# Optimization experiments

Measured on AMD Instinct MI355X. Metric: run time of the kernel, lower is better.

The kernel has to match this reference:

```python
import jax, jax.numpy as jnp
import numpy as np
import math

MAX_P = 150
D_MODEL = 128
N_HEADS = 4
D_HEAD = D_MODEL // N_HEADS
D_MLP = 512
D_MEM = 64
VOCAB = MAX_P + 2  # 152
EQ_TOKEN = MAX_P + 1  # 151
B = 65536


def setup_inputs() -> dict:
    key = jax.random.key(0)
    ks = jax.random.split(key, 20)
    s = 1.0 / math.sqrt(D_MODEL)
    inp = {
        "p_val": jax.random.randint(ks[0], (B,), 0, MAX_P),
        "a": jax.random.randint(ks[1], (B,), 0, MAX_P),
        "b": jax.random.randint(ks[2], (B,), 0, MAX_P),
        # embeddings
        "token_embed": jax.random.normal(ks[3], (VOCAB, D_MODEL), jnp.float32),
        "pos_embed": jax.random.normal(ks[4], (5, D_MODEL), jnp.float32),
        # TitansMemory
        "W_mem": jax.random.normal(ks[5], (D_MODEL, D_MEM), jnp.float32) * s,
        "b_mem": jnp.zeros((D_MEM,), jnp.float32),
        "W_sur": jax.random.normal(ks[6], (D_MEM, D_MODEL), jnp.float32) * (1.0 / math.sqrt(D_MEM)),
        "b_sur": jnp.zeros((D_MODEL,), jnp.float32),
        "W_m2r": jax.random.normal(ks[7], (D_MEM, D_MODEL), jnp.float32) * (1.0 / math.sqrt(D_MEM)),
        "b_m2r": jnp.zeros((D_MODEL,), jnp.float32),
        # attention
        "W_Q": jax.random.normal(ks[8], (N_HEADS, D_MODEL, D_HEAD), jnp.float32) * s,
        "W_K": jax.random.normal(ks[9], (N_HEADS, D_MODEL, D_HEAD), jnp.float32) * s,
        "W_V": jax.random.normal(ks[10], (N_HEADS, D_MODEL, D_HEAD), jnp.float32) * s,
        "W_O": jax.random.normal(ks[11], (N_HEADS, D_HEAD, D_MODEL), jnp.float32) * s,
        # MLP
        "W_mlp1": jax.random.normal(ks[12], (D_MODEL, D_MLP), jnp.float32) * s,
        "b_mlp1": jnp.zeros((D_MLP,), jnp.float32),
        "W_mlp2": jax.random.normal(ks[13], (D_MLP, D_MODEL), jnp.float32) * (1.0 / math.sqrt(D_MLP)),
        "b_mlp2": jnp.zeros((D_MODEL,), jnp.float32),
        # unembed
        "W_un": jax.random.normal(ks[14], (D_MODEL, MAX_P), jnp.float32) * s,
        "b_un": jnp.zeros((MAX_P,), jnp.float32),
    }
    return inp


def reference(p_val, a, b, token_embed, pos_embed, W_mem, b_mem, W_sur, b_sur,
              W_m2r, b_m2r, W_Q, W_K, W_V, W_O, W_mlp1, b_mlp1, W_mlp2, b_mlp2,
              W_un, b_un):
    eq = jnp.full_like(a, EQ_TOKEN)
    tokens = jnp.stack([p_val, a, b, eq], axis=1)            # [B, 4]
    x = token_embed[tokens] + pos_embed[:4][None, :, :]       # [B, 4, D]

    # Titans memory (test-time update) on the modulus token embedding
    x0 = x[:, 0, :]                                           # [B, D]
    z = jax.nn.silu(x0 @ W_mem + b_mem)                       # [B, d_mem]
    pred_x = z @ W_sur + b_sur                                # [B, D]
    update = jax.nn.silu((x0 - pred_x) @ W_mem)               # [B, d_mem]
    mem = (z + update) @ W_m2r + b_m2r                        # [B, D]
    x = x + mem[:, None, :]

    # attention
    q = jnp.einsum('bsd,hdk->bhsk', x, W_Q)
    k = jnp.einsum('bsd,hdk->bhsk', x, W_K)
    v = jnp.einsum('bsd,hdk->bhsk', x, W_V)
    scores = jnp.einsum('bhsk,bhtk->bhst', q, k) / math.sqrt(D_HEAD)
    pattern = jax.nn.softmax(scores, axis=-1)                 # [B, H, 4, 4]
    attn = jnp.einsum('bhst,bhtk->bhsk', pattern, v)
    attn = jnp.einsum('bhsk,hkm->bsm', attn, W_O)             # [B, 4, D]
    x = x + attn

    # MLP
    x = x + jax.nn.relu(x @ W_mlp1 + b_mlp1) @ W_mlp2 + b_mlp2

    # unembed the '=' position
    logits = x[:, 3, :] @ W_un + b_un                         # [B, max_p]
    return logits
```

## Files before the change

kernel.cpp:

```cpp
#include <hip/hip_runtime.h>

#define D      128
#define DM     64
#define DMLP   512
#define PMAX   150
#define VOC    152
#define EQT    151
#define NBATCH 65536

typedef __attribute__((ext_vector_type(8))) __bf16 bf16x8;
typedef __attribute__((ext_vector_type(4))) float  f32x4;

__device__ __forceinline__ float silu_f(float x){ return x / (1.0f + expf(-x)); }

#define OFF_MEMVEC 0
#define OFF_X3BASE 19200
#define OFF_KE     19328
#define OFF_KP     38784
#define OFF_SC     39296
#define OFF_O0     132896
#define OFF_O1     171296
#define OFF_O2     209696
#define OFF_O3     248096
#define OFF_M3B    248352
#define OFF_W1F    257952
#define OFF_W2F    290720
#define OFF_WUF    323488

__global__ void k_P1(const float* __restrict__ tok, const float* __restrict__ pos,
                     const float* __restrict__ W_mem, const float* __restrict__ b_mem,
                     const float* __restrict__ W_sur, const float* __restrict__ b_sur,
                     const float* __restrict__ W_m2r, const float* __restrict__ b_m2r,
                     const float* __restrict__ W_K, const float* __restrict__ W_V,
                     const float* __restrict__ W_O,
                     const float* __restrict__ W1, const float* __restrict__ W2,
                     const float* __restrict__ WU,
                     float* __restrict__ memvec, float* __restrict__ x3base,
                     float* __restrict__ KE, float* __restrict__ KP,
                     __bf16* __restrict__ O0, __bf16* __restrict__ O1,
                     __bf16* __restrict__ O2, __bf16* __restrict__ O3,
                     __bf16* __restrict__ W1f, __bf16* __restrict__ W2f, __bf16* __restrict__ WUf)
{
    int r = blockIdx.x, t = threadIdx.x;
    if (r < 150) {
        int p = r;
        __shared__ float sx0[D], sz[DM], sdiff[D], szu[DM];
        if (t < D) sx0[t] = tok[p*D + t] + pos[t];
        __syncthreads();
        if (t < DM) {
            float acc = b_mem[t];
            for (int d = 0; d < D; d++) acc += sx0[d] * W_mem[d*DM + t];
            sz[t] = silu_f(acc);
        }
        __syncthreads();
        if (t < D) {
            float acc = b_sur[t];
            for (int j = 0; j < DM; j++) acc += sz[j] * W_sur[j*D + t];
            sdiff[t] = sx0[t] - acc;
        }
        __syncthreads();
        if (t < DM) {
            float acc = 0.f;
            for (int d = 0; d < D; d++) acc += sdiff[d] * W_mem[d*DM + t];
            szu[t] = sz[t] + silu_f(acc);
        }
        __syncthreads();
        if (t < D) {
            float acc = b_m2r[t];
            for (int j = 0; j < DM; j++) acc += szu[j] * W_m2r[j*D + t];
            memvec[p*D + t] = acc;
        }
    } else if (r == 150) {
        if (t < D) x3base[t] = tok[EQT*D + t] + pos[3*D + t];
    } else if (r < 307) {
        int idx = r - 151;
        const float* src = (idx < 152) ? (tok + idx*D) : (pos + (idx-152)*D);
        float*       dst = (idx < 152) ? (KE + idx*D)  : (KP + (idx-152)*D);
        __shared__ float s[D];
        if (t < D) s[t] = src[t];
        __syncthreads();
        if (t < D) {
            int h = t >> 5, k = t & 31;
            float acc = 0.f;
            for (int d = 0; d < D; d++) acc += s[d] * W_K[h*4096 + d*32 + k];
            dst[t] = acc;
        }
    } else if (r < 758) {
        int idx = r - 307;
        int tt, v; __bf16* outp;
        if (idx < 150)      { tt = 0; v = idx;       outp = O0 + v*512; }
        else if (idx < 300) { tt = 1; v = idx - 150; outp = O1 + (idx-150)*512; }
        else if (idx < 450) { tt = 2; v = idx - 300; outp = O2 + (idx-300)*512; }
        else                { tt = 3; v = EQT;       outp = O3; }
        __shared__ float sTP[D], sv[D];
        if (t < D) sTP[t] = tok[v*D + t] + pos[tt*D + t];
        __syncthreads();
        if (t < D) {
            int h = t >> 5, k = t & 31;
            float acc = 0.f;
            for (int d = 0; d < D; d++) acc += sTP[d] * W_V[h*4096 + d*32 + k];
            sv[t] = acc;
        }
        __syncthreads();
        #pragma unroll
        for (int i = 0; i < 2; i++) {
            int c = t + i*256;
            int h = c >> 7, m = c & 127;
            float acc = 0.f;
            for (int k = 0; k < 32; k++) acc += sv[h*32 + k] * W_O[h*4096 + k*128 + m];
            outp[c] = (__bf16)acc;
        }
    } else if (r < 790) {
        int f = (r-758)*256 + t;
        int l = f & 63, kb = (f>>6) & 3, nb = f >> 8;
        int k0 = kb*32 + (l>>4)*8, n = nb*16 + (l&15);
        #pragma unroll
        for (int j = 0; j < 8; j++) W1f[f*8 + j] = (__bf16)W1[(k0+j)*DMLP + n];
    } else if (r < 822) {
        int f = (r-790)*256 + t;
        int l = f & 63, g = f >> 6;
        int nb = g & 7, kb = g >> 3;
        int k0 = kb*32 + (l>>4)*8, n = nb*16 + (l&15);
        #pragma unroll
        for (int j = 0; j < 8; j++) W2f[f*8 + j] = (__bf16)W2[(k0+j)*D + n];
    } else {
        int f = (r-822)*256 + t;
        int l = f & 63, kb = (f>>6) & 3, nb = f >> 8;
        int k0 = kb*32 + (l>>4)*8, n = nb*16 + (l&15);
        #pragma unroll
        for (int j = 0; j < 8; j++) WUf[f*8 + j] = (__bf16)((n < 150) ? WU[(k0+j)*150 + n] : 0.f);
    }
}

__global__ void k_P2(const float* __restrict__ memvec, const float* __restrict__ x3base,
                     const float* __restrict__ W_Q, const float* __restrict__ W_V,
                     const float* __restrict__ W_O,
                     const float* __restrict__ KE, const float* __restrict__ KP,
                     float* __restrict__ SC, __bf16* __restrict__ M3B)
{
    int r = blockIdx.x, p = r >> 1, half = r & 1, t = threadIdx.x;
    __shared__ float sMem[D], sIn[D], sQ3[D], sMV[D];
    if (t < D) { float m = memvec[p*D + t]; sMem[t] = m; sIn[t] = m + x3base[t]; }
    __syncthreads();
    if (t < D) {
        int h = t >> 5, k = t & 31;
        float acc = 0.f;
        for (int d = 0; d < D; d++) acc += sIn[d] * W_Q[h*4096 + d*32 + k];
        sQ3[t] = acc;
    } else {
        int c = t - D; int h = c >> 5, k = c & 31;
        float acc = 0.f;
        for (int d = 0; d < D; d++) acc += sMem[d] * W_V[h*4096 + d*32 + k];
        sMV[c] = acc;
    }
    __syncthreads();
    const float scale = 0.17677669529663687f;
    for (int ii = t; ii < 312; ii += 256) {
        int i = half*312 + ii;
        int v = i >> 2, h = i & 3;
        const float4* qh = (const float4*)(sQ3 + h*32);
        float4 s4 = {0.f, 0.f, 0.f, 0.f};
        if (v < 152) {
            const float4* ke = (const float4*)(KE + v*D + h*32);
            #pragma unroll
            for (int k = 0; k < 8; k++) {
                float4 q = qh[k], e = ke[k];
                s4.x += q.x*e.x; s4.y += q.y*e.y; s4.z += q.z*e.z; s4.w += q.w*e.w;
            }
        } else if (v == 152 || v == 153) {
            const float4* ke = (const float4*)(KE + ((v==152)? p : EQT)*D + h*32);
            const float4* kp = (const float4*)(KP + ((v==152)? 0 : 3)*D + h*32);
            #pragma unroll
            for (int k = 0; k < 8; k++) {
                float4 q = qh[k], e = ke[k], pp = kp[k];
                s4.x += q.x*(e.x+pp.x); s4.y += q.y*(e.y+pp.y);
                s4.z += q.z*(e.z+pp.z); s4.w += q.w*(e.w+pp.w);
            }
        } else {
            const float4* kp = (const float4*)(KP + ((v==154)?1:2)*D + h*32);
            #pragma unroll
            for (int k = 0; k < 8; k++) {
                float4 q = qh[k], pp = kp[k];
                s4.x += q.x*pp.x; s4.y += q.y*pp.y; s4.z += q.z*pp.z; s4.w += q.w*pp.w;
            }
        }
        SC[p*624 + i] = (s4.x + s4.y + s4.z + s4.w) * scale;
    }
    if (half == 0 && t < D) {
        float acc = sIn[t];
        for (int c = 0; c < D; c++) acc += sMV[c] * W_O[c*D + t];
        M3B[p*D + t] = (__bf16)acc;
    }
}

__global__ __launch_bounds__(256, 4) void k_fused(
    const int* __restrict__ p_val, const int* __restrict__ a_tok, const int* __restrict__ b_tok,
    const float* __restrict__ SC, const __bf16* __restrict__ O0, const __bf16* __restrict__ O1,
    const __bf16* __restrict__ O2, const __bf16* __restrict__ O3g, const __bf16* __restrict__ M3B,
    const __bf16* __restrict__ W1f, const __bf16* __restrict__ W2f, const __bf16* __restrict__ WUf,
    const float* __restrict__ b1, const float* __restrict__ b2, const float* __restrict__ bun,
    float* __restrict__ out)
{
    __shared__ __align__(16) char smem[36992];
    float* sB = (float*)(smem + 33792);
    char* sX3 = smem + 16384;

    int tid = threadIdx.x;
    int wv = tid >> 6, l = tid & 63, lr = l & 15, quad = l >> 4;
    int tbase = blockIdx.x * 64 + wv * 16;

    const char* gW1 = (const char*)W1f;
    const char* gW2 = (const char*)W2f;

    float4 v0, v1, v2, v3;
    {
        const float4* g1 = (const float4*)(gW1) + tid*2;
        const float4* g2 = (const float4*)(gW2) + tid*2;
        v0 = g1[0]; v1 = g1[1]; v2 = g2[0]; v3 = g2[1];
    }

    for (int i = tid; i < 512; i += 256) sB[i] = b1[i];
    if (tid < 128) sB[512 + tid] = b2[tid];
    if (tid < 160) sB[640 + tid] = bun[tid];

    {
        int s = tid >> 2, h = tid & 3;
        int gs = blockIdx.x * 64 + s;
        int p = p_val[gs], ta = a_tok[gs], tb = b_tok[gs];

        float wloc[4];
        {
            const float* SCp = SC + p*624;
            float sc0 = SCp[608 + h];
            float sc3 = SCp[612 + h];
            float sc1 = SCp[ta*4 + h] + SCp[616 + h];
            float sc2 = SCp[tb*4 + h] + SCp[620 + h];
            float mx = fmaxf(fmaxf(sc0, sc1), fmaxf(sc2, sc3));
            float e0 = expf(sc0-mx), e1 = expf(sc1-mx), e2 = expf(sc2-mx), e3 = expf(sc3-mx);
            float inv = 1.f / (e0 + e1 + e2 + e3);
            wloc[0] = e0*inv; wloc[1] = e1*inv; wloc[2] = e2*inv; wloc[3] = e3*inv;
        }
        float w[16];
        #pragma unroll
        for (int j = 0; j < 4; j++) w[h*4 + j] = wloc[j];
        #pragma unroll
        for (int m = 1; m < 4; m++) {
            int oh = h ^ m;
            #pragma unroll
            for (int j = 0; j < 4; j++) w[oh*4 + j] = __shfl_xor(wloc[j], m);
        }

        const bf16x8* m3v = (const bf16x8*)(M3B + p*128);
        const bf16x8* t0  = (const bf16x8*)(O0 + p*512);
        const bf16x8* t1  = (const bf16x8*)(O1 + ta*512);
        const bf16x8* t2  = (const bf16x8*)(O2 + tb*512);
        const bf16x8* t3  = (const bf16x8*)O3g;
        #pragma unroll
        for (int jj = 0; jj < 4; jj++) {
            int c8 = h*4 + jj;
            bf16x8 mv = m3v[c8];
            float v[8];
            #pragma unroll
            for (int e = 0; e < 8; e++) v[e] = (float)mv[e];
            #pragma unroll
            for (int hh = 0; hh < 4; hh++) {
                int o8 = hh*16 + c8;
                bf16x8 e0 = t0[o8], e1 = t1[o8], e2 = t2[o8], e3 = t3[o8];
                float w0 = w[hh*4+0], w1 = w[hh*4+1], w2 = w[hh*4+2], w3 = w[hh*4+3];
                #pragma unroll
                for (int e = 0; e < 8; e++)
                    v[e] += w0*(float)e0[e] + w1*(float)e1[e] + w2*(float)e2[e] + w3*(float)e3[e];
            }
            bf16x8 st;
            #pragma unroll
            for (int e = 0; e < 8; e++) st[e] = (__bf16)v[e];
            *(bf16x8*)(sX3 + s*256 + ((c8*16) ^ ((s&7)<<4))) = st;
        }
    }
    __syncthreads();

    bf16x8 a[4];
    {
        int arow = wv*16 + lr;
        #pragma unroll
        for (int kb = 0; kb < 4; kb++)
            a[kb] = *(const bf16x8*)(sX3 + arow*256 + ((kb*64 + quad*16) ^ ((lr&7)<<4)));
    }

    char* sPanC = smem + 16384 + wv*1280;

    f32x4 acc2[8];
    #pragma unroll
    for (int i = 0; i < 8; i++) acc2[i] = (f32x4){0.f, 0.f, 0.f, 0.f};

    for (int cc = 0; cc < 16; cc++) {
        {
            float4* d1 = (float4*)(smem) + tid*2;
            float4* d2 = (float4*)(smem + 8192) + tid*2;
            d1[0] = v0; d1[1] = v1; d2[0] = v2; d2[1] = v3;
        }
        __syncthreads();
        if (cc < 15) {
            const float4* g1 = (const float4*)(gW1 + (cc+1)*8192) + tid*2;
            const float4* g2 = (const float4*)(gW2 + (cc+1)*8192) + tid*2;
            v0 = g1[0]; v1 = g1[1]; v2 = g2[0]; v3 = g2[1];
        }
        #pragma unroll
        for (int nbl = 0; nbl < 2; nbl++) {
            float bv = sB[cc*32 + nbl*16 + lr];
            f32x4 acc = (f32x4){bv, bv, bv, bv};
            #pragma unroll
            for (int kb = 0; kb < 4; kb++) {
                bf16x8 w1 = *(const bf16x8*)(smem + ((nbl*4 + kb)*64 + l)*16);
                acc = __builtin_amdgcn_mfma_f32_16x16x32_bf16(a[kb], w1, acc, 0, 0, 0);
            }
            #pragma unroll
            for (int r = 0; r < 4; r++)
                *(__bf16*)(sPanC + (((quad*4 + r)*40) + nbl*16 + lr)*2) = (__bf16)fmaxf(acc[r], 0.f);
        }
        {
            bf16x8 h = *(const bf16x8*)(sPanC + (lr*40 + quad*8)*2);
            #pragma unroll
            for (int nb2 = 0; nb2 < 8; nb2++) {
                bf16x8 w2 = *(const bf16x8*)(smem + 8192 + (nb2*64 + l)*16);
                acc2[nb2] = __builtin_amdgcn_mfma_f32_16x16x32_bf16(h, w2, acc2[nb2], 0, 0, 0);
            }
        }
        __syncthreads();
    }

    #pragma unroll
    for (int nb2 = 0; nb2 < 8; nb2++) {
        int kb = nb2 >> 1;
        bf16x8 bi;
        #pragma unroll
        for (int j = 0; j < 8; j++)
            bi[j] = (kb*32 + quad*8 + j == nb2*16 + lr) ? (__bf16)1.0f : (__bf16)0.0f;
        acc2[nb2] = __builtin_amdgcn_mfma_f32_16x16x32_bf16(a[kb], bi, acc2[nb2], 0, 0, 0);
    }

    char* sPanE = smem + 16384 + wv*4352;
    #pragma unroll
    for (int nb2 = 0; nb2 < 8; nb2++) {
        int n = nb2*16 + lr;
        float bv = sB[512 + n];
        #pragma unroll
        for (int r = 0; r < 4; r++) {
            float v = acc2[nb2][r] + bv;
            *(__bf16*)(sPanE + (((quad*4 + r)*136) + n)*2) = (__bf16)v;
        }
    }
    bf16x8 au[4];
    #pragma unroll
    for (int kb = 0; kb < 4; kb++)
        au[kb] = *(const bf16x8*)(sPanE + (lr*136 + kb*32 + quad*8)*2);

    const char* gWU = (const char*)WUf;
    #pragma unroll
    for (int q = 0; q < 3; q++) {
        if (q < 2) {
            const float4* g = (const float4*)(gWU + q*16384) + tid*4;
            float4 u0 = g[0], u1 = g[1], u2 = g[2], u3 = g[3];
            float4* dd = (float4*)(smem) + tid*4;
            dd[0] = u0; dd[1] = u1; dd[2] = u2; dd[3] = u3;
        } else {
            const float4* g = (const float4*)(gWU + 32768) + tid*2;
            float4 u0 = g[0], u1 = g[1];
            float4* dd = (float4*)(smem) + tid*2;
            dd[0] = u0; dd[1] = u1;
        }
        __syncthreads();
        int ntn = (q < 2) ? 4 : 2;
        for (int ntl = 0; ntl < ntn; ntl++) {
            int nt = q*4 + ntl;
            int n = nt*16 + lr;
            float bv = (n < 150) ? sB[640 + n] : 0.f;
            f32x4 acc = (f32x4){bv, bv, bv, bv};
            #pragma unroll
            for (int kb = 0; kb < 4; kb++) {
                bf16x8 wu = *(const bf16x8*)(smem + ((ntl*4 + kb)*64 + l)*16);
                acc = __builtin_amdgcn_mfma_f32_16x16x32_bf16(au[kb], wu, acc, 0, 0, 0);
            }
            if (n < 150) {
                #pragma unroll
                for (int r = 0; r < 4; r++) {
                    int rowg = tbase + quad*4 + r;
                    out[rowg*150 + n] = acc[r];
                }
            }
        }
        if (q < 2) __syncthreads();
    }
}

extern "C" void kernel_launch(void* const* d_in, const int* in_sizes, int n_in,
                              void* d_out, int out_size, void* d_ws, size_t ws_size,
                              hipStream_t stream) {
    const int*   p_val = (const int*)d_in[0];
    const int*   a_tok = (const int*)d_in[1];
    const int*   b_tok = (const int*)d_in[2];
    const float* tok   = (const float*)d_in[3];
    const float* pos   = (const float*)d_in[4];
    const float* W_mem = (const float*)d_in[5];
    const float* b_mem = (const float*)d_in[6];
    const float* W_sur = (const float*)d_in[7];
    const float* b_sur = (const float*)d_in[8];
    const float* W_m2r = (const float*)d_in[9];
    const float* b_m2r = (const float*)d_in[10];
    const float* W_Q   = (const float*)d_in[11];
    const float* W_K   = (const float*)d_in[12];
    const float* W_V   = (const float*)d_in[13];
    const float* W_O   = (const float*)d_in[14];
    const float* W1    = (const float*)d_in[15];
    const float* b1    = (const float*)d_in[16];
    const float* W2    = (const float*)d_in[17];
    const float* b2    = (const float*)d_in[18];
    const float* WU    = (const float*)d_in[19];
    const float* bun   = (const float*)d_in[20];
    float* out = (float*)d_out;

    float* ws = (float*)d_ws;
    float* memvec = ws + OFF_MEMVEC;
    float* x3base = ws + OFF_X3BASE;
    float* KE     = ws + OFF_KE;
    float* KP     = ws + OFF_KP;
    float* SC     = ws + OFF_SC;
    __bf16* O0    = (__bf16*)(ws + OFF_O0);
    __bf16* O1    = (__bf16*)(ws + OFF_O1);
    __bf16* O2    = (__bf16*)(ws + OFF_O2);
    __bf16* O3    = (__bf16*)(ws + OFF_O3);
    __bf16* M3B   = (__bf16*)(ws + OFF_M3B);
    __bf16* W1f   = (__bf16*)(ws + OFF_W1F);
    __bf16* W2f   = (__bf16*)(ws + OFF_W2F);
    __bf16* WUf   = (__bf16*)(ws + OFF_WUF);

    k_P1<<<832, 256, 0, stream>>>(tok, pos, W_mem, b_mem, W_sur, b_sur, W_m2r, b_m2r,
                                  W_K, W_V, W_O, W1, W2, WU,
                                  memvec, x3base, KE, KP, O0, O1, O2, O3, W1f, W2f, WUf);
    k_P2<<<300, 256, 0, stream>>>(memvec, x3base, W_Q, W_V, W_O, KE, KP, SC, M3B);
    k_fused<<<NBATCH/64, 256, 0, stream>>>(p_val, a_tok, b_tok, SC, O0, O1, O2, O3, M3B,
                                           W1f, W2f, WUf, b1, b2, bun, out);
}
```

Before: 183.2 us.

## Double rows per block in fused MLP kernel and rebalance precompute kernels

The main kernel now handles 128 rows per block (32 per wave, two MFMA row groups), so each staged W1/W2/WU tile is reused across twice as many rows and weight streaming is halved. Shared memory grows and launch bounds drop to 2 blocks per SM to leave room for the extra registers. Weight tile copies now use strided per-thread float4 indexing for coalesced access. The precompute kernels are regrouped so the value/W_O and weight-format work runs alongside the score computation in the second kernel, shortening the first kernel's critical path.

```diff
diff --git a/kernel.cpp b/kernel.cpp
--- a/kernel.cpp
+++ b/kernel.cpp
@@ -27,19 +27,13 @@
 #define OFF_W2F    290720
 #define OFF_WUF    323488
 
-__global__ void k_P1(const float* __restrict__ tok, const float* __restrict__ pos,
-                     const float* __restrict__ W_mem, const float* __restrict__ b_mem,
-                     const float* __restrict__ W_sur, const float* __restrict__ b_sur,
-                     const float* __restrict__ W_m2r, const float* __restrict__ b_m2r,
-                     const float* __restrict__ W_K, const float* __restrict__ W_V,
-                     const float* __restrict__ W_O,
-                     const float* __restrict__ W1, const float* __restrict__ W2,
-                     const float* __restrict__ WU,
-                     float* __restrict__ memvec, float* __restrict__ x3base,
-                     float* __restrict__ KE, float* __restrict__ KP,
-                     __bf16* __restrict__ O0, __bf16* __restrict__ O1,
-                     __bf16* __restrict__ O2, __bf16* __restrict__ O3,
-                     __bf16* __restrict__ W1f, __bf16* __restrict__ W2f, __bf16* __restrict__ WUf)
+__global__ void k_P1a(const float* __restrict__ tok, const float* __restrict__ pos,
+                      const float* __restrict__ W_mem, const float* __restrict__ b_mem,
+                      const float* __restrict__ W_sur, const float* __restrict__ b_sur,
+                      const float* __restrict__ W_m2r, const float* __restrict__ b_m2r,
+                      const float* __restrict__ W_K,
+                      float* __restrict__ memvec, float* __restrict__ x3base,
+                      float* __restrict__ KE, float* __restrict__ KP)
 {
     int r = blockIdx.x, t = threadIdx.x;
     if (r < 150) {
@@ -72,7 +66,7 @@
         }
     } else if (r == 150) {
         if (t < D) x3base[t] = tok[EQT*D + t] + pos[3*D + t];
-    } else if (r < 307) {
+    } else {
         int idx = r - 151;
         const float* src = (idx < 152) ? (tok + idx*D) : (pos + (idx-152)*D);
         float*       dst = (idx < 152) ? (KE + idx*D)  : (KP + (idx-152)*D);
@@ -85,8 +79,81 @@
             for (int d = 0; d < D; d++) acc += s[d] * W_K[h*4096 + d*32 + k];
             dst[t] = acc;
         }
-    } else if (r < 758) {
-        int idx = r - 307;
+    }
+}
+
+__global__ void k_P2x(const float* __restrict__ memvec, const float* __restrict__ x3base,
+                      const float* __restrict__ W_Q, const float* __restrict__ W_V,
+                      const float* __restrict__ W_O,
+                      const float* __restrict__ KE, const float* __restrict__ KP,
+                      const float* __restrict__ tok, const float* __restrict__ pos,
+                      const float* __restrict__ W1, const float* __restrict__ W2,
+                      const float* __restrict__ WU,
+                      float* __restrict__ SC, __bf16* __restrict__ M3B,
+                      __bf16* __restrict__ O0, __bf16* __restrict__ O1,
+                      __bf16* __restrict__ O2, __bf16* __restrict__ O3,
+                      __bf16* __restrict__ W1f, __bf16* __restrict__ W2f, __bf16* __restrict__ WUf)
+{
+    int r = blockIdx.x, t = threadIdx.x;
+    if (r < 300) {
+        int p = r >> 1, half = r & 1;
+        __shared__ float sMem[D], sIn[D], sQ3[D], sMV[D];
+        if (t < D) { float m = memvec[p*D + t]; sMem[t] = m; sIn[t] = m + x3base[t]; }
+        __syncthreads();
+        if (t < D) {
+            int h = t >> 5, k = t & 31;
+            float acc = 0.f;
+            for (int d = 0; d < D; d++) acc += sIn[d] * W_Q[h*4096 + d*32 + k];
+            sQ3[t] = acc;
+        } else {
+            int c = t - D; int h = c >> 5, k = c & 31;
+            float acc = 0.f;
+            for (int d = 0; d < D; d++) acc += sMem[d] * W_V[h*4096 + d*32 + k];
+            sMV[c] = acc;
+        }
+        __syncthreads();
+        const float scale = 0.17677669529663687f;
+        for (int ii = t; ii < 312; ii += 256) {
+            int i = half*312 + ii;
+            int v = i >> 2, h = i & 3;
+            const float4* qh = (const float4*)(sQ3 + h*32);
+            float4 s4 = {0.f, 0.f, 0.f, 0.f};
+            if (v < 152) {
+                const float4* ke = (const float4*)(KE + v*D + h*32);
+                #pragma unroll
+                for (int k = 0; k < 8; k++) {
+                    float4 q = qh[k], e = ke[k];
+                    s4.x += q.x*e.x; s4.y += q.y*e.y; s4.z += q.z*e.z; s4.w += q.w*e.w;
+                }
+            } else if (v == 152 || v == 153) {
+                const float4* ke = (const float4*)(KE + ((v==152)? p : EQT)*D + h*32);
+                const float4* kp = (const float4*)(KP + ((v==152)? 0 : 3)*D + h*32);
+                #pragma unroll
+                for (int k = 0; k < 8; k++) {
+                    float4 q = qh[k], e = ke[k], pp = kp[k];
+                    s4.x += q.x*(e.x+pp.x); s4.y += q.y*(e.y+pp.y);
+                    s4.z += q.z*(e.z+pp.z); s4.w += q.w*(e.w+pp.w);
+                }
+            } else {
+                const float4* kp = (const float4*)(KP + ((v==154)?1:2)*D + h*32);
+                #pragma unroll
+                for (int k = 0; k < 8; k++) {
+                    float4 q = qh[k], pp = kp[k];
+                    s4.x += q.x*pp.x; s4.y += q.y*pp.y; s4.z += q.z*pp.z; s4.w += q.w*pp.w;
+                }
+            }
+            SC[p*624 + i] = (s4.x + s4.y + s4.z + s4.w) * scale;
+        }
+        if (half == 0 && t < D) {
+            float acc = sIn[t];
+            for (int c = 0; c < D; c++) acc += sMV[c] * W_O[c*D + t];
+            M3B[p*D + t] = (__bf16)acc;
+        }
+        return;
+    }
+    int rr = r - 300;
+    if (rr < 451) {
+        int idx = rr;
         int tt, v; __bf16* outp;
         if (idx < 150)      { tt = 0; v = idx;       outp = O0 + v*512; }
         else if (idx < 300) { tt = 1; v = idx - 150; outp = O1 + (idx-150)*512; }
@@ -110,21 +177,21 @@
             for (int k = 0; k < 32; k++) acc += sv[h*32 + k] * W_O[h*4096 + k*128 + m];
             outp[c] = (__bf16)acc;
         }
-    } else if (r < 790) {
-        int f = (r-758)*256 + t;
+    } else if (rr < 483) {
+        int f = (rr-451)*256 + t;
         int l = f & 63, kb = (f>>6) & 3, nb = f >> 8;
         int k0 = kb*32 + (l>>4)*8, n = nb*16 + (l&15);
         #pragma unroll
         for (int j = 0; j < 8; j++) W1f[f*8 + j] = (__bf16)W1[(k0+j)*DMLP + n];
-    } else if (r < 822) {
-        int f = (r-790)*256 + t;
+    } else if (rr < 515) {
+        int f = (rr-483)*256 + t;
         int l = f & 63, g = f >> 6;
         int nb = g & 7, kb = g >> 3;
         int k0 = kb*32 + (l>>4)*8, n = nb*16 + (l&15);
         #pragma unroll
         for (int j = 0; j < 8; j++) W2f[f*8 + j] = (__bf16)W2[(k0+j)*D + n];
     } else {
-        int f = (r-822)*256 + t;
+        int f = (rr-515)*256 + t;
         int l = f & 63, kb = (f>>6) & 3, nb = f >> 8;
         int k0 = kb*32 + (l>>4)*8, n = nb*16 + (l&15);
         #pragma unroll
@@ -132,68 +199,7 @@
     }
 }
 
-__global__ void k_P2(const float* __restrict__ memvec, const float* __restrict__ x3base,
-                     const float* __restrict__ W_Q, const float* __restrict__ W_V,
-                     const float* __restrict__ W_O,
-                     const float* __restrict__ KE, const float* __restrict__ KP,
-                     float* __restrict__ SC, __bf16* __restrict__ M3B)
-{
-    int r = blockIdx.x, p = r >> 1, half = r & 1, t = threadIdx.x;
-    __shared__ float sMem[D], sIn[D], sQ3[D], sMV[D];
-    if (t < D) { float m = memvec[p*D + t]; sMem[t] = m; sIn[t] = m + x3base[t]; }
-    __syncthreads();
-    if (t < D) {
-        int h = t >> 5, k = t & 31;
-        float acc = 0.f;
-        for (int d = 0; d < D; d++) acc += sIn[d] * W_Q[h*4096 + d*32 + k];
-        sQ3[t] = acc;
-    } else {
-        int c = t - D; int h = c >> 5, k = c & 31;
-        float acc = 0.f;
-        for (int d = 0; d < D; d++) acc += sMem[d] * W_V[h*4096 + d*32 + k];
-        sMV[c] = acc;
-    }
-    __syncthreads();
-    const float scale = 0.17677669529663687f;
-    for (int ii = t; ii < 312; ii += 256) {
-        int i = half*312 + ii;
-        int v = i >> 2, h = i & 3;
-        const float4* qh = (const float4*)(sQ3 + h*32);
-        float4 s4 = {0.f, 0.f, 0.f, 0.f};
-        if (v < 152) {
-            const float4* ke = (const float4*)(KE + v*D + h*32);
-            #pragma unroll
-            for (int k = 0; k < 8; k++) {
-                float4 q = qh[k], e = ke[k];
-                s4.x += q.x*e.x; s4.y += q.y*e.y; s4.z += q.z*e.z; s4.w += q.w*e.w;
-            }
-        } else if (v == 152 || v == 153) {
-            const float4* ke = (const float4*)(KE + ((v==152)? p : EQT)*D + h*32);
-            const float4* kp = (const float4*)(KP + ((v==152)? 0 : 3)*D + h*32);
-            #pragma unroll
-            for (int k = 0; k < 8; k++) {
-                float4 q = qh[k], e = ke[k], pp = kp[k];
-                s4.x += q.x*(e.x+pp.x); s4.y += q.y*(e.y+pp.y);
-                s4.z += q.z*(e.z+pp.z); s4.w += q.w*(e.w+pp.w);
-            }
-        } else {
-            const float4* kp = (const float4*)(KP + ((v==154)?1:2)*D + h*32);
-            #pragma unroll
-            for (int k = 0; k < 8; k++) {
-                float4 q = qh[k], pp = kp[k];
-                s4.x += q.x*pp.x; s4.y += q.y*pp.y; s4.z += q.z*pp.z; s4.w += q.w*pp.w;
-            }
-        }
-        SC[p*624 + i] = (s4.x + s4.y + s4.z + s4.w) * scale;
-    }
-    if (half == 0 && t < D) {
-        float acc = sIn[t];
-        for (int c = 0; c < D; c++) acc += sMV[c] * W_O[c*D + t];
-        M3B[p*D + t] = (__bf16)acc;
-    }
-}
-
-__global__ __launch_bounds__(256, 4) void k_fused(
+__global__ __launch_bounds__(256, 2) void k_fused(
     const int* __restrict__ p_val, const int* __restrict__ a_tok, const int* __restrict__ b_tok,
     const float* __restrict__ SC, const __bf16* __restrict__ O0, const __bf16* __restrict__ O1,
     const __bf16* __restrict__ O2, const __bf16* __restrict__ O3g, const __bf16* __restrict__ M3B,
@@ -201,31 +207,32 @@
     const float* __restrict__ b1, const float* __restrict__ b2, const float* __restrict__ bun,
     float* __restrict__ out)
 {
-    __shared__ __align__(16) char smem[36992];
-    float* sB = (float*)(smem + 33792);
-    char* sX3 = smem + 16384;
+    __shared__ __align__(16) char smem[54400];
+    float* sB = (float*)(smem + 51200);
+    char* sX3 = smem;
 
     int tid = threadIdx.x;
     int wv = tid >> 6, l = tid & 63, lr = l & 15, quad = l >> 4;
-    int tbase = blockIdx.x * 64 + wv * 16;
+    int tbase = blockIdx.x * 128 + wv * 32;
 
     const char* gW1 = (const char*)W1f;
     const char* gW2 = (const char*)W2f;
 
     float4 v0, v1, v2, v3;
     {
-        const float4* g1 = (const float4*)(gW1) + tid*2;
-        const float4* g2 = (const float4*)(gW2) + tid*2;
-        v0 = g1[0]; v1 = g1[1]; v2 = g2[0]; v3 = g2[1];
+        const float4* g1 = (const float4*)gW1;
+        const float4* g2 = (const float4*)gW2;
+        v0 = g1[tid]; v1 = g1[tid + 256]; v2 = g2[tid]; v3 = g2[tid + 256];
     }
 
     for (int i = tid; i < 512; i += 256) sB[i] = b1[i];
     if (tid < 128) sB[512 + tid] = b2[tid];
     if (tid < 160) sB[640 + tid] = bun[tid];
 
-    {
-        int s = tid >> 2, h = tid & 3;
-        int gs = blockIdx.x * 64 + s;
+    #pragma unroll
+    for (int ss = 0; ss < 2; ss++) {
+        int s = (tid >> 2) + ss*64, h = tid & 3;
+        int gs = blockIdx.x * 128 + s;
         int p = p_val[gs], ta = a_tok[gs], tb = b_tok[gs];
 
         float wloc[4];
@@ -279,51 +286,61 @@
     }
     __syncthreads();
 
-    bf16x8 a[4];
-    {
-        int arow = wv*16 + lr;
+    bf16x8 a[2][4];
+    #pragma unroll
+    for (int rg = 0; rg < 2; rg++) {
+        int arow = wv*32 + rg*16 + lr;
         #pragma unroll
         for (int kb = 0; kb < 4; kb++)
-            a[kb] = *(const bf16x8*)(sX3 + arow*256 + ((kb*64 + quad*16) ^ ((lr&7)<<4)));
-    }
-
-    char* sPanC = smem + 16384 + wv*1280;
-
-    f32x4 acc2[8];
-    #pragma unroll
-    for (int i = 0; i < 8; i++) acc2[i] = (f32x4){0.f, 0.f, 0.f, 0.f};
+            a[rg][kb] = *(const bf16x8*)(sX3 + arow*256 + ((kb*64 + quad*16) ^ ((lr&7)<<4)));
+    }
+    __syncthreads();
+
+    char* sPanC = smem + 16384 + wv*2560;
+
+    f32x4 acc2[2][8];
+    #pragma unroll
+    for (int rg = 0; rg < 2; rg++)
+        #pragma unroll
+        for (int i = 0; i < 8; i++) acc2[rg][i] = (f32x4){0.f, 0.f, 0.f, 0.f};
 
     for (int cc = 0; cc < 16; cc++) {
         {
-            float4* d1 = (float4*)(smem) + tid*2;
-            float4* d2 = (float4*)(smem + 8192) + tid*2;
-            d1[0] = v0; d1[1] = v1; d2[0] = v2; d2[1] = v3;
+            float4* d1 = (float4*)smem;
+            float4* d2 = (float4*)(smem + 8192);
+            d1[tid] = v0; d1[tid + 256] = v1; d2[tid] = v2; d2[tid + 256] = v3;
         }
         __syncthreads();
         if (cc < 15) {
-            const float4* g1 = (const float4*)(gW1 + (cc+1)*8192) + tid*2;
-            const float4* g2 = (const float4*)(gW2 + (cc+1)*8192) + tid*2;
-            v0 = g1[0]; v1 = g1[1]; v2 = g2[0]; v3 = g2[1];
+            const float4* g1 = (const float4*)(gW1 + (cc+1)*8192);
+            const float4* g2 = (const float4*)(gW2 + (cc+1)*8192);
+            v0 = g1[tid]; v1 = g1[tid + 256]; v2 = g2[tid]; v3 = g2[tid + 256];
         }
         #pragma unroll
         for (int nbl = 0; nbl < 2; nbl++) {
             float bv = sB[cc*32 + nbl*16 + lr];
-            f32x4 acc = (f32x4){bv, bv, bv, bv};
+            f32x4 accA = (f32x4){bv, bv, bv, bv};
+            f32x4 accB = (f32x4){bv, bv, bv, bv};
             #pragma unroll
             for (int kb = 0; kb < 4; kb++) {
                 bf16x8 w1 = *(const bf16x8*)(smem + ((nbl*4 + kb)*64 + l)*16);
-                acc = __builtin_amdgcn_mfma_f32_16x16x32_bf16(a[kb], w1, acc, 0, 0, 0);
-            }
-            #pragma unroll
-            for (int r = 0; r < 4; r++)
-                *(__bf16*)(sPanC + (((quad*4 + r)*40) + nbl*16 + lr)*2) = (__bf16)fmaxf(acc[r], 0.f);
+                accA = __builtin_amdgcn_mfma_f32_16x16x32_bf16(a[0][kb], w1, accA, 0, 0, 0);
+                accB = __builtin_amdgcn_mfma_f32_16x16x32_bf16(a[1][kb], w1, accB, 0, 0, 0);
+            }
+            #pragma unroll
+            for (int r = 0; r < 4; r++) {
+                *(__bf16*)(sPanC + (((quad*4 + r)*40)      + nbl*16 + lr)*2) = (__bf16)fmaxf(accA[r], 0.f);
+                *(__bf16*)(sPanC + (((16 + quad*4 + r)*40) + nbl*16 + lr)*2) = (__bf16)fmaxf(accB[r], 0.f);
+            }
         }
         {
-            bf16x8 h = *(const bf16x8*)(sPanC + (lr*40 + quad*8)*2);
+            bf16x8 h0 = *(const bf16x8*)(sPanC + ((lr)*40      + quad*8)*2);
+            bf16x8 h1 = *(const bf16x8*)(sPanC + ((16 + lr)*40 + quad*8)*2);
             #pragma unroll
             for (int nb2 = 0; nb2 < 8; nb2++) {
                 bf16x8 w2 = *(const bf16x8*)(smem + 8192 + (nb2*64 + l)*16);
-                acc2[nb2] = __builtin_amdgcn_mfma_f32_16x16x32_bf16(h, w2, acc2[nb2], 0, 0, 0);
+                acc2[0][nb2] = __builtin_amdgcn_mfma_f32_16x16x32_bf16(h0, w2, acc2[0][nb2], 0, 0, 0);
+                acc2[1][nb2] = __builtin_amdgcn_mfma_f32_16x16x32_bf16(h1, w2, acc2[1][nb2], 0, 0, 0);
             }
         }
         __syncthreads();
@@ -336,38 +353,43 @@
         #pragma unroll
         for (int j = 0; j < 8; j++)
             bi[j] = (kb*32 + quad*8 + j == nb2*16 + lr) ? (__bf16)1.0f : (__bf16)0.0f;
-        acc2[nb2] = __builtin_amdgcn_mfma_f32_16x16x32_bf16(a[kb], bi, acc2[nb2], 0, 0, 0);
-    }
-
-    char* sPanE = smem + 16384 + wv*4352;
+        acc2[0][nb2] = __builtin_amdgcn_mfma_f32_16x16x32_bf16(a[0][kb], bi, acc2[0][nb2], 0, 0, 0);
+        acc2[1][nb2] = __builtin_amdgcn_mfma_f32_16x16x32_bf16(a[1][kb], bi, acc2[1][nb2], 0, 0, 0);
+    }
+
+    char* sPanE = smem + 16384 + wv*8704;
     #pragma unroll
     for (int nb2 = 0; nb2 < 8; nb2++) {
         int n = nb2*16 + lr;
         float bv = sB[512 + n];
         #pragma unroll
-        for (int r = 0; r < 4; r++) {
-            float v = acc2[nb2][r] + bv;
-            *(__bf16*)(sPanE + (((quad*4 + r)*136) + n)*2) = (__bf16)v;
-        }
-    }
-    bf16x8 au[4];
-    #pragma unroll
-    for (int kb = 0; kb < 4; kb++)
-        au[kb] = *(const bf16x8*)(sPanE + (lr*136 + kb*32 + quad*8)*2);
+        for (int rg = 0; rg < 2; rg++)
+            #pragma unroll
+            for (int r = 0; r < 4; r++) {
+                float v = acc2[rg][nb2][r] + bv;
+                *(__bf16*)(sPanE + (((rg*16 + quad*4 + r)*136) + n)*2) = (__bf16)v;
+            }
+    }
+    bf16x8 au[2][4];
+    #pragma unroll
+    for (int rg = 0; rg < 2; rg++)
+        #pragma unroll
+        for (int kb = 0; kb < 4; kb++)
+            au[rg][kb] = *(const bf16x8*)(sPanE + ((rg*16 + lr)*136 + kb*32 + quad*8)*2);
 
     const char* gWU = (const char*)WUf;
     #pragma unroll
     for (int q = 0; q < 3; q++) {
         if (q < 2) {
-            const float4* g = (const float4*)(gWU + q*16384) + tid*4;
-            float4 u0 = g[0], u1 = g[1], u2 = g[2], u3 = g[3];
-            float4* dd = (float4*)(smem) + tid*4;
-            dd[0] = u0; dd[1] = u1; dd[2] = u2; dd[3] = u3;
+            const float4* g = (const float4*)(gWU + q*16384);
+            float4 u0 = g[tid], u1 = g[tid+256], u2 = g[tid+512], u3 = g[tid+768];
+            float4* dd = (float4*)smem;
+            dd[tid] = u0; dd[tid+256] = u1; dd[tid+512] = u2; dd[tid+768] = u3;
         } else {
-            const float4* g = (const float4*)(gWU + 32768) + tid*2;
-            float4 u0 = g[0], u1 = g[1];
-            float4* dd = (float4*)(smem) + tid*2;
-            dd[0] = u0; dd[1] = u1;
+            const float4* g = (const float4*)(gWU + 32768);
+            float4 u0 = g[tid], u1 = g[tid+256];
+            float4* dd = (float4*)smem;
+            dd[tid] = u0; dd[tid+256] = u1;
         }
         __syncthreads();
         int ntn = (q < 2) ? 4 : 2;
@@ -375,17 +397,19 @@
             int nt = q*4 + ntl;
             int n = nt*16 + lr;
             float bv = (n < 150) ? sB[640 + n] : 0.f;
-            f32x4 acc = (f32x4){bv, bv, bv, bv};
+            f32x4 accU0 = (f32x4){bv, bv, bv, bv};
+            f32x4 accU1 = (f32x4){bv, bv, bv, bv};
             #pragma unroll
             for (int kb = 0; kb < 4; kb++) {
                 bf16x8 wu = *(const bf16x8*)(smem + ((ntl*4 + kb)*64 + l)*16);
-                acc = __builtin_amdgcn_mfma_f32_16x16x32_bf16(au[kb], wu, acc, 0, 0, 0);
+                accU0 = __builtin_amdgcn_mfma_f32_16x16x32_bf16(au[0][kb], wu, accU0, 0, 0, 0);
+                accU1 = __builtin_amdgcn_mfma_f32_16x16x32_bf16(au[1][kb], wu, accU1, 0, 0, 0);
             }
             if (n < 150) {
                 #pragma unroll
                 for (int r = 0; r < 4; r++) {
-                    int rowg = tbase + quad*4 + r;
-                    out[rowg*150 + n] = acc[r];
+                    out[(tbase +      quad*4 + r)*150 + n] = accU0[r];
+                    out[(tbase + 16 + quad*4 + r)*150 + n] = accU1[r];
                 }
             }
         }
@@ -434,10 +458,11 @@
     __bf16* W2f   = (__bf16*)(ws + OFF_W2F);
     __bf16* WUf   = (__bf16*)(ws + OFF_WUF);
 
-    k_P1<<<832, 256, 0, stream>>>(tok, pos, W_mem, b_mem, W_sur, b_sur, W_m2r, b_m2r,
-                                  W_K, W_V, W_O, W1, W2, WU,
-                                  memvec, x3base, KE, KP, O0, O1, O2, O3, W1f, W2f, WUf);
-    k_P2<<<300, 256, 0, stream>>>(memvec, x3base, W_Q, W_V, W_O, KE, KP, SC, M3B);
-    k_fused<<<NBATCH/64, 256, 0, stream>>>(p_val, a_tok, b_tok, SC, O0, O1, O2, O3, M3B,
-                                           W1f, W2f, WUf, b1, b2, bun, out);
+    k_P1a<<<307, 256, 0, stream>>>(tok, pos, W_mem, b_mem, W_sur, b_sur, W_m2r, b_m2r,
+                                   W_K, memvec, x3base, KE, KP);
+    k_P2x<<<825, 256, 0, stream>>>(memvec, x3base, W_Q, W_V, W_O, KE, KP,
+                                   tok, pos, W1, W2, WU,
+                                   SC, M3B, O0, O1, O2, O3, W1f, W2f, WUf);
+    k_fused<<<NBATCH/128, 256, 0, stream>>>(p_val, a_tok, b_tok, SC, O0, O1, O2, O3, M3B,
+                                            W1f, W2f, WUf, b1, b2, bun, out);
 }
```

Result: faster. 179.3 us (-2.2%).

## Rebalance precompute kernels and coalesce weight-tile global loads

Applied to the files above, without the earlier changes.

Moves the independent value/output-projection tables and the bf16 weight-fragment repacking out of the first precompute kernel and into the second, so the first kernel shrinks to the memory/key work that the second depends on. This shortens the serialized critical path across the two dependent launches. It also changes the per-thread float4 indexing of the weight tile copies in the main fused kernel from tid*2/tid*4 strides to tid + k*256 strides, so adjacent lanes touch adjacent 16-byte chunks for coalesced global loads and conflict-free LDS stores. Each thread copies a different set of chunks, but together the threads still copy the same full tile.

```diff
diff --git a/kernel.cpp b/kernel.cpp
--- a/kernel.cpp
+++ b/kernel.cpp
@@ -27,19 +27,13 @@
 #define OFF_W2F    290720
 #define OFF_WUF    323488
 
-__global__ void k_P1(const float* __restrict__ tok, const float* __restrict__ pos,
-                     const float* __restrict__ W_mem, const float* __restrict__ b_mem,
-                     const float* __restrict__ W_sur, const float* __restrict__ b_sur,
-                     const float* __restrict__ W_m2r, const float* __restrict__ b_m2r,
-                     const float* __restrict__ W_K, const float* __restrict__ W_V,
-                     const float* __restrict__ W_O,
-                     const float* __restrict__ W1, const float* __restrict__ W2,
-                     const float* __restrict__ WU,
-                     float* __restrict__ memvec, float* __restrict__ x3base,
-                     float* __restrict__ KE, float* __restrict__ KP,
-                     __bf16* __restrict__ O0, __bf16* __restrict__ O1,
-                     __bf16* __restrict__ O2, __bf16* __restrict__ O3,
-                     __bf16* __restrict__ W1f, __bf16* __restrict__ W2f, __bf16* __restrict__ WUf)
+__global__ void k_P1a(const float* __restrict__ tok, const float* __restrict__ pos,
+                      const float* __restrict__ W_mem, const float* __restrict__ b_mem,
+                      const float* __restrict__ W_sur, const float* __restrict__ b_sur,
+                      const float* __restrict__ W_m2r, const float* __restrict__ b_m2r,
+                      const float* __restrict__ W_K,
+                      float* __restrict__ memvec, float* __restrict__ x3base,
+                      float* __restrict__ KE, float* __restrict__ KP)
 {
     int r = blockIdx.x, t = threadIdx.x;
     if (r < 150) {
@@ -72,7 +66,7 @@
         }
     } else if (r == 150) {
         if (t < D) x3base[t] = tok[EQT*D + t] + pos[3*D + t];
-    } else if (r < 307) {
+    } else {
         int idx = r - 151;
         const float* src = (idx < 152) ? (tok + idx*D) : (pos + (idx-152)*D);
         float*       dst = (idx < 152) ? (KE + idx*D)  : (KP + (idx-152)*D);
@@ -85,8 +79,81 @@
             for (int d = 0; d < D; d++) acc += s[d] * W_K[h*4096 + d*32 + k];
             dst[t] = acc;
         }
-    } else if (r < 758) {
-        int idx = r - 307;
+    }
+}
+
+__global__ void k_P2x(const float* __restrict__ memvec, const float* __restrict__ x3base,
+                      const float* __restrict__ W_Q, const float* __restrict__ W_V,
+                      const float* __restrict__ W_O,
+                      const float* __restrict__ KE, const float* __restrict__ KP,
+                      const float* __restrict__ tok, const float* __restrict__ pos,
+                      const float* __restrict__ W1, const float* __restrict__ W2,
+                      const float* __restrict__ WU,
+                      float* __restrict__ SC, __bf16* __restrict__ M3B,
+                      __bf16* __restrict__ O0, __bf16* __restrict__ O1,
+                      __bf16* __restrict__ O2, __bf16* __restrict__ O3,
+                      __bf16* __restrict__ W1f, __bf16* __restrict__ W2f, __bf16* __restrict__ WUf)
+{
+    int r = blockIdx.x, t = threadIdx.x;
+    if (r < 300) {
+        int p = r >> 1, half = r & 1;
+        __shared__ float sMem[D], sIn[D], sQ3[D], sMV[D];
+        if (t < D) { float m = memvec[p*D + t]; sMem[t] = m; sIn[t] = m + x3base[t]; }
+        __syncthreads();
+        if (t < D) {
+            int h = t >> 5, k = t & 31;
+            float acc = 0.f;
+            for (int d = 0; d < D; d++) acc += sIn[d] * W_Q[h*4096 + d*32 + k];
+            sQ3[t] = acc;
+        } else {
+            int c = t - D; int h = c >> 5, k = c & 31;
+            float acc = 0.f;
+            for (int d = 0; d < D; d++) acc += sMem[d] * W_V[h*4096 + d*32 + k];
+            sMV[c] = acc;
+        }
+        __syncthreads();
+        const float scale = 0.17677669529663687f;
+        for (int ii = t; ii < 312; ii += 256) {
+            int i = half*312 + ii;
+            int v = i >> 2, h = i & 3;
+            const float4* qh = (const float4*)(sQ3 + h*32);
+            float4 s4 = {0.f, 0.f, 0.f, 0.f};
+            if (v < 152) {
+                const float4* ke = (const float4*)(KE + v*D + h*32);
+                #pragma unroll
+                for (int k = 0; k < 8; k++) {
+                    float4 q = qh[k], e = ke[k];
+                    s4.x += q.x*e.x; s4.y += q.y*e.y; s4.z += q.z*e.z; s4.w += q.w*e.w;
+                }
+            } else if (v == 152 || v == 153) {
+                const float4* ke = (const float4*)(KE + ((v==152)? p : EQT)*D + h*32);
+                const float4* kp = (const float4*)(KP + ((v==152)? 0 : 3)*D + h*32);
+                #pragma unroll
+                for (int k = 0; k < 8; k++) {
+                    float4 q = qh[k], e = ke[k], pp = kp[k];
+                    s4.x += q.x*(e.x+pp.x); s4.y += q.y*(e.y+pp.y);
+                    s4.z += q.z*(e.z+pp.z); s4.w += q.w*(e.w+pp.w);
+                }
+            } else {
+                const float4* kp = (const float4*)(KP + ((v==154)?1:2)*D + h*32);
+                #pragma unroll
+                for (int k = 0; k < 8; k++) {
+                    float4 q = qh[k], pp = kp[k];
+                    s4.x += q.x*pp.x; s4.y += q.y*pp.y; s4.z += q.z*pp.z; s4.w += q.w*pp.w;
+                }
+            }
+            SC[p*624 + i] = (s4.x + s4.y + s4.z + s4.w) * scale;
+        }
+        if (half == 0 && t < D) {
+            float acc = sIn[t];
+            for (int c = 0; c < D; c++) acc += sMV[c] * W_O[c*D + t];
+            M3B[p*D + t] = (__bf16)acc;
+        }
+        return;
+    }
+    int rr = r - 300;
+    if (rr < 451) {
+        int idx = rr;
         int tt, v; __bf16* outp;
         if (idx < 150)      { tt = 0; v = idx;       outp = O0 + v*512; }
         else if (idx < 300) { tt = 1; v = idx - 150; outp = O1 + (idx-150)*512; }
@@ -110,86 +177,25 @@
             for (int k = 0; k < 32; k++) acc += sv[h*32 + k] * W_O[h*4096 + k*128 + m];
             outp[c] = (__bf16)acc;
         }
-    } else if (r < 790) {
-        int f = (r-758)*256 + t;
+    } else if (rr < 483) {
+        int f = (rr-451)*256 + t;
         int l = f & 63, kb = (f>>6) & 3, nb = f >> 8;
         int k0 = kb*32 + (l>>4)*8, n = nb*16 + (l&15);
         #pragma unroll
         for (int j = 0; j < 8; j++) W1f[f*8 + j] = (__bf16)W1[(k0+j)*DMLP + n];
-    } else if (r < 822) {
-        int f = (r-790)*256 + t;
+    } else if (rr < 515) {
+        int f = (rr-483)*256 + t;
         int l = f & 63, g = f >> 6;
         int nb = g & 7, kb = g >> 3;
         int k0 = kb*32 + (l>>4)*8, n = nb*16 + (l&15);
         #pragma unroll
         for (int j = 0; j < 8; j++) W2f[f*8 + j] = (__bf16)W2[(k0+j)*D + n];
     } else {
-        int f = (r-822)*256 + t;
+        int f = (rr-515)*256 + t;
         int l = f & 63, kb = (f>>6) & 3, nb = f >> 8;
         int k0 = kb*32 + (l>>4)*8, n = nb*16 + (l&15);
         #pragma unroll
         for (int j = 0; j < 8; j++) WUf[f*8 + j] = (__bf16)((n < 150) ? WU[(k0+j)*150 + n] : 0.f);
-    }
-}
-
-__global__ void k_P2(const float* __restrict__ memvec, const float* __restrict__ x3base,
-                     const float* __restrict__ W_Q, const float* __restrict__ W_V,
-                     const float* __restrict__ W_O,
-                     const float* __restrict__ KE, const float* __restrict__ KP,
-                     float* __restrict__ SC, __bf16* __restrict__ M3B)
-{
-    int r = blockIdx.x, p = r >> 1, half = r & 1, t = threadIdx.x;
-    __shared__ float sMem[D], sIn[D], sQ3[D], sMV[D];
-    if (t < D) { float m = memvec[p*D + t]; sMem[t] = m; sIn[t] = m + x3base[t]; }
-    __syncthreads();
-    if (t < D) {
-        int h = t >> 5, k = t & 31;
-        float acc = 0.f;
-        for (int d = 0; d < D; d++) acc += sIn[d] * W_Q[h*4096 + d*32 + k];
-        sQ3[t] = acc;
-    } else {
-        int c = t - D; int h = c >> 5, k = c & 31;
-        float acc = 0.f;
-        for (int d = 0; d < D; d++) acc += sMem[d] * W_V[h*4096 + d*32 + k];
-        sMV[c] = acc;
-    }
-    __syncthreads();
-    const float scale = 0.17677669529663687f;
-    for (int ii = t; ii < 312; ii += 256) {
-        int i = half*312 + ii;
-        int v = i >> 2, h = i & 3;
-        const float4* qh = (const float4*)(sQ3 + h*32);
-        float4 s4 = {0.f, 0.f, 0.f, 0.f};
-        if (v < 152) {
-            const float4* ke = (const float4*)(KE + v*D + h*32);
-            #pragma unroll
-            for (int k = 0; k < 8; k++) {
-                float4 q = qh[k], e = ke[k];
-                s4.x += q.x*e.x; s4.y += q.y*e.y; s4.z += q.z*e.z; s4.w += q.w*e.w;
-            }
-        } else if (v == 152 || v == 153) {
-            const float4* ke = (const float4*)(KE + ((v==152)? p : EQT)*D + h*32);
-            const float4* kp = (const float4*)(KP + ((v==152)? 0 : 3)*D + h*32);
-            #pragma unroll
-            for (int k = 0; k < 8; k++) {
-                float4 q = qh[k], e = ke[k], pp = kp[k];
-                s4.x += q.x*(e.x+pp.x); s4.y += q.y*(e.y+pp.y);
-                s4.z += q.z*(e.z+pp.z); s4.w += q.w*(e.w+pp.w);
-            }
-        } else {
-            const float4* kp = (const float4*)(KP + ((v==154)?1:2)*D + h*32);
-            #pragma unroll
-            for (int k = 0; k < 8; k++) {
-                float4 q = qh[k], pp = kp[k];
-                s4.x += q.x*pp.x; s4.y += q.y*pp.y; s4.z += q.z*pp.z; s4.w += q.w*pp.w;
-            }
-        }
-        SC[p*624 + i] = (s4.x + s4.y + s4.z + s4.w) * scale;
-    }
-    if (half == 0 && t < D) {
-        float acc = sIn[t];
-        for (int c = 0; c < D; c++) acc += sMV[c] * W_O[c*D + t];
-        M3B[p*D + t] = (__bf16)acc;
     }
 }
 
@@ -214,9 +220,9 @@
 
     float4 v0, v1, v2, v3;
     {
-        const float4* g1 = (const float4*)(gW1) + tid*2;
-        const float4* g2 = (const float4*)(gW2) + tid*2;
-        v0 = g1[0]; v1 = g1[1]; v2 = g2[0]; v3 = g2[1];
+        const float4* g1 = (const float4*)gW1;
+        const float4* g2 = (const float4*)gW2;
+        v0 = g1[tid]; v1 = g1[tid + 256]; v2 = g2[tid]; v3 = g2[tid + 256];
     }
 
     for (int i = tid; i < 512; i += 256) sB[i] = b1[i];
@@ -295,15 +301,15 @@
 
     for (int cc = 0; cc < 16; cc++) {
         {
-            float4* d1 = (float4*)(smem) + tid*2;
-            float4* d2 = (float4*)(smem + 8192) + tid*2;
-            d1[0] = v0; d1[1] = v1; d2[0] = v2; d2[1] = v3;
+            float4* d1 = (float4*)smem;
+            float4* d2 = (float4*)(smem + 8192);
+            d1[tid] = v0; d1[tid + 256] = v1; d2[tid] = v2; d2[tid + 256] = v3;
         }
         __syncthreads();
         if (cc < 15) {
-            const float4* g1 = (const float4*)(gW1 + (cc+1)*8192) + tid*2;
-            const float4* g2 = (const float4*)(gW2 + (cc+1)*8192) + tid*2;
-            v0 = g1[0]; v1 = g1[1]; v2 = g2[0]; v3 = g2[1];
+            const float4* g1 = (const float4*)(gW1 + (cc+1)*8192);
+            const float4* g2 = (const float4*)(gW2 + (cc+1)*8192);
+            v0 = g1[tid]; v1 = g1[tid + 256]; v2 = g2[tid]; v3 = g2[tid + 256];
         }
         #pragma unroll
         for (int nbl = 0; nbl < 2; nbl++) {
@@ -359,15 +365,15 @@
     #pragma unroll
     for (int q = 0; q < 3; q++) {
         if (q < 2) {
-            const float4* g = (const float4*)(gWU + q*16384) + tid*4;
-            float4 u0 = g[0], u1 = g[1], u2 = g[2], u3 = g[3];
-            float4* dd = (float4*)(smem) + tid*4;
-            dd[0] = u0; dd[1] = u1; dd[2] = u2; dd[3] = u3;
+            const float4* g = (const float4*)(gWU + q*16384);
+            float4 u0 = g[tid], u1 = g[tid+256], u2 = g[tid+512], u3 = g[tid+768];
+            float4* dd = (float4*)smem;
+            dd[tid] = u0; dd[tid+256] = u1; dd[tid+512] = u2; dd[tid+768] = u3;
         } else {
-            const float4* g = (const float4*)(gWU + 32768) + tid*2;
-            float4 u0 = g[0], u1 = g[1];
-            float4* dd = (float4*)(smem) + tid*2;
-            dd[0] = u0; dd[1] = u1;
+            const float4* g = (const float4*)(gWU + 32768);
+            float4 u0 = g[tid], u1 = g[tid+256];
+            float4* dd = (float4*)smem;
+            dd[tid] = u0; dd[tid+256] = u1;
         }
         __syncthreads();
         int ntn = (q < 2) ? 4 : 2;
@@ -434,10 +440,11 @@
     __bf16* W2f   = (__bf16*)(ws + OFF_W2F);
     __bf16* WUf   = (__bf16*)(ws + OFF_WUF);
 
-    k_P1<<<832, 256, 0, stream>>>(tok, pos, W_mem, b_mem, W_sur, b_sur, W_m2r, b_m2r,
-                                  W_K, W_V, W_O, W1, W2, WU,
-                                  memvec, x3base, KE, KP, O0, O1, O2, O3, W1f, W2f, WUf);
-    k_P2<<<300, 256, 0, stream>>>(memvec, x3base, W_Q, W_V, W_O, KE, KP, SC, M3B);
+    k_P1a<<<307, 256, 0, stream>>>(tok, pos, W_mem, b_mem, W_sur, b_sur, W_m2r, b_m2r,
+                                   W_K, memvec, x3base, KE, KP);
+    k_P2x<<<825, 256, 0, stream>>>(memvec, x3base, W_Q, W_V, W_O, KE, KP,
+                                   tok, pos, W1, W2, WU,
+                                   SC, M3B, O0, O1, O2, O3, W1f, W2f, WUf);
     k_fused<<<NBATCH/64, 256, 0, stream>>>(p_val, a_tok, b_tok, SC, O0, O1, O2, O3, M3B,
                                            W1f, W2f, WUf, b1, b2, bun, out);
 }
```

Result: no change. 182.9 us (-0.2%).
